# Kernel optimization log

Measured on AMD Instinct MI355X. Metric: run time of the kernel, lower is better.

Reference implementation:

```python
import jax, jax.numpy as jnp
import numpy as np


def setup_inputs() -> dict:
    key = jax.random.key(0)
    kq, kk, kv = jax.random.split(key, 3)
    B, H, S, D = 4, 16, 2048, 64
    q = jax.random.normal(kq, (B, H, S, D), dtype=jnp.float32)
    k = jax.random.normal(kk, (B, H, S, D), dtype=jnp.float32)
    v = jax.random.normal(kv, (B, H, S, D), dtype=jnp.float32)
    return {"q": q, "k": k, "v": v}


def reference(q, k, v):
    # SplitScaleAttend (inference, no mask, no dropout):
    # softmax(q k^T / sqrt(d)) v — the chunked loop in the original is a
    # memory-saving schedule of the same math, so one fused expression here.
    scale = q.shape[-1] ** (-0.5)
    # (b h i d),(b h j d) -> (b h i j)
    sim = jnp.einsum("bhid,bhjd->bhij", q, k * scale)
    attn = jax.nn.softmax(sim, axis=-1)
    # (b h i j),(b h j d) -> (b h i d)
    return jnp.einsum("bhij,bhjd->bhid", attn, v)
```

## Files before the change

kernel.cpp:

```cpp
#include <hip/hip_runtime.h>
#include <hip/hip_bf16.h>

typedef __attribute__((ext_vector_type(8))) short short8_t;
typedef __attribute__((ext_vector_type(4))) float f32x4;
typedef __attribute__((ext_vector_type(16))) float f32x16;
typedef __attribute__((ext_vector_type(4))) unsigned u32x4;

static constexpr int B = 4, H = 16, S = 2048, D = 64;
static constexpr int WAVES = 8, QW = 32, QBLK = WAVES * QW;
static constexpr int KVBLK = 64, NT = S / KVBLK;
static constexpr int LDK = 72;

#define QSCALE 0.18033688011112042f

__device__ __forceinline__ unsigned pk2(float a, float b) {
    __hip_bfloat162 h = __float22bfloat162_rn(float2{a, b});
    unsigned u;
    __builtin_memcpy(&u, &h, 4);
    return u;
}

__device__ __forceinline__ float fexp2(float x) {
#if __has_builtin(__builtin_amdgcn_exp2f)
    return __builtin_amdgcn_exp2f(x);
#else
    return exp2f(x);
#endif
}

__device__ __forceinline__ float frcp(float x) {
#if __has_builtin(__builtin_amdgcn_rcpf)
    return __builtin_amdgcn_rcpf(x);
#else
    return 1.f / x;
#endif
}

#define PV_STEP(CD, H, KS)                                                               \
    do {                                                                                 \
        unsigned x0 = CD[4 * (H) + 0], y0 = CD[4 * (H) + 2];                             \
        unsigned x1 = CD[4 * (H) + 1], y1 = CD[4 * (H) + 3];                             \
        asm volatile("v_permlane32_swap_b32 %0, %1" : "+v"(x0), "+v"(y0));               \
        asm volatile("v_permlane32_swap_b32 %0, %1" : "+v"(x1), "+v"(y1));               \
        const u32x4 pu = {x0, x1, y0, y1};                                               \
        const short8_t pa = __builtin_bit_cast(short8_t, pu);                            \
        const short8_t vfa =                                                             \
            *reinterpret_cast<const short8_t*>(&Vt[cb][ql][(KS) * 16 + hi * 8]);         \
        const short8_t vfb =                                                             \
            *reinterpret_cast<const short8_t*>(&Vt[cb][32 + ql][(KS) * 16 + hi * 8]);    \
        Od0 = __builtin_amdgcn_mfma_f32_32x32x16_bf16(pa, vfa, Od0, 0, 0, 0);            \
        Od1 = __builtin_amdgcn_mfma_f32_32x32x16_bf16(pa, vfb, Od1, 0, 0, 0);            \
        Ol  = __builtin_amdgcn_mfma_f32_32x32x16_bf16(pa, onesf, Ol, 0, 0, 0);           \
    } while (0)

__global__ void __launch_bounds__(512, 2)
attn_fwd(const float* __restrict__ q, const float* __restrict__ k,
         const float* __restrict__ v, float* __restrict__ out) {
    __shared__ short Ks[2][KVBLK][LDK];
    __shared__ short Vt[2][D][LDK];

    const int tid  = threadIdx.x;
    const int lane = tid & 63;
    const int ql   = lane & 31;
    const int hi   = lane >> 5;
    const int wave = tid >> 6;

    const long base = (long)blockIdx.y * S * D;
    const int  q0w  = blockIdx.x * QBLK + wave * QW;

    const u32x4 ones_u = {0x3F803F80u, 0x3F803F80u, 0x3F803F80u, 0x3F803F80u};
    const short8_t onesf = __builtin_bit_cast(short8_t, ones_u);

    short8_t qf[4];
    {
        const float* qp = q + base + (long)(q0w + ql) * D;
        #pragma unroll
        for (int kc = 0; kc < 4; ++kc) {
            const f32x4 a = *reinterpret_cast<const f32x4*>(qp + kc * 16 + hi * 8);
            const f32x4 b = *reinterpret_cast<const f32x4*>(qp + kc * 16 + hi * 8 + 4);
            const u32x4 u = {pk2(a[0] * QSCALE, a[1] * QSCALE),
                             pk2(a[2] * QSCALE, a[3] * QSCALE),
                             pk2(b[0] * QSCALE, b[1] * QSCALE),
                             pk2(b[2] * QSCALE, b[3] * QSCALE)};
            qf[kc] = __builtin_bit_cast(short8_t, u);
        }
    }

    f32x16 Od0, Od1, Ol;
    #pragma unroll
    for (int r = 0; r < 16; ++r) { Od0[r] = 0.f; Od1[r] = 0.f; Ol[r] = 0.f; }

    const int kr  = tid >> 3,       kc0 = (tid & 7) * 8;
    const int vk2 = (tid & 31) * 2, vd0 = (tid >> 5) * 4;
    const float* kptr  = k + base + (long)kr * D + kc0;
    const float* vptrA = v + base + (long)vk2 * D + vd0;
    const float* vptrB = vptrA + D;

    f32x4 kf0 = *reinterpret_cast<const f32x4*>(kptr);
    f32x4 kf1 = *reinterpret_cast<const f32x4*>(kptr + 4);
    f32x4 vfA = *reinterpret_cast<const f32x4*>(vptrA);
    f32x4 vfB = *reinterpret_cast<const f32x4*>(vptrB);

    for (int t = 0; t < NT; ++t) {
        const int cb = t & 1;
        {
            const u32x4 ku = {pk2(kf0[0], kf0[1]), pk2(kf0[2], kf0[3]),
                              pk2(kf1[0], kf1[1]), pk2(kf1[2], kf1[3])};
            *reinterpret_cast<u32x4*>(&Ks[cb][kr][kc0]) = ku;
            #pragma unroll
            for (int j = 0; j < 4; ++j) {
                const unsigned uv = pk2(vfA[j], vfB[j]);
                *reinterpret_cast<unsigned*>(&Vt[cb][vd0 + j][vk2]) = uv;
            }
        }
        if (t + 1 < NT) {
            kptr  += KVBLK * D;
            vptrA += KVBLK * D;
            vptrB += KVBLK * D;
            kf0 = *reinterpret_cast<const f32x4*>(kptr);
            kf1 = *reinterpret_cast<const f32x4*>(kptr + 4);
            vfA = *reinterpret_cast<const f32x4*>(vptrA);
            vfB = *reinterpret_cast<const f32x4*>(vptrB);
        }
        __syncthreads();

        f32x16 sA, sB;
        #pragma unroll
        for (int r = 0; r < 16; ++r) { sA[r] = 0.f; sB[r] = 0.f; }
        __builtin_amdgcn_s_setprio(1);
        #pragma unroll
        for (int kc = 0; kc < 4; ++kc) {
            const short8_t ka = *reinterpret_cast<const short8_t*>(&Ks[cb][ql][kc * 16 + hi * 8]);
            sA = __builtin_amdgcn_mfma_f32_32x32x16_bf16(ka, qf[kc], sA, 0, 0, 0);
        }
        #pragma unroll
        for (int kc = 0; kc < 4; ++kc) {
            const short8_t kb2 = *reinterpret_cast<const short8_t*>(&Ks[cb][32 + ql][kc * 16 + hi * 8]);
            sB = __builtin_amdgcn_mfma_f32_32x32x16_bf16(kb2, qf[kc], sB, 0, 0, 0);
        }
        __builtin_amdgcn_s_setprio(0);

        #pragma unroll
        for (int r = 0; r < 16; ++r) sA[r] = fexp2(sA[r]);
        #pragma unroll
        for (int r = 0; r < 16; ++r) sB[r] = fexp2(sB[r]);

        unsigned cdA[8], cdB[8];
        #pragma unroll
        for (int jj = 0; jj < 8; ++jj) {
            cdA[jj] = pk2(sA[jj * 2], sA[jj * 2 + 1]);
            cdB[jj] = pk2(sB[jj * 2], sB[jj * 2 + 1]);
        }

        __builtin_amdgcn_s_setprio(1);
        PV_STEP(cdA, 0, 0);
        PV_STEP(cdA, 1, 1);
        PV_STEP(cdB, 0, 2);
        PV_STEP(cdB, 1, 3);
        __builtin_amdgcn_s_setprio(0);
    }

    float* op = out + base + (long)q0w * D + ql;
    #pragma unroll
    for (int r = 0; r < 16; ++r) {
        const int   row = (r & 3) + 8 * (r >> 2) + 4 * hi;
        const float s   = frcp(Ol[r]);
        op[(long)row * D]      = Od0[r] * s;
        op[(long)row * D + 32] = Od1[r] * s;
    }
}

extern "C" void kernel_launch(void* const* d_in, const int* in_sizes, int n_in,
                              void* d_out, int out_size, void* d_ws, size_t ws_size,
                              hipStream_t stream) {
    const float* q = (const float*)d_in[0];
    const float* k = (const float*)d_in[1];
    const float* v = (const float*)d_in[2];
    float* out = (float*)d_out;
    dim3 grid(S / QBLK, B * H);
    attn_fwd<<<grid, 512, 0, stream>>>(q, k, v, out);
}
```

Baseline: 104.6 us.

## Process two 32-row query tiles per wave with four waves per block

Each wave now owns 64 query rows as two 32-row MFMA tiles, so each K and V fragment read from LDS is reused for both tiles, and the block drops to four waves. The loop is reordered so the next tile's global K/V loads are issued after the first QK half, and the QK/exp/PV work is split into two halves per KV tile. This halves LDS fragment traffic per query row and blocks per head stay the same. In exchange each wave holds twice as many accumulators, which raises register pressure, and there are fewer waves to hide latency.

```diff
diff --git a/kernel.cpp b/kernel.cpp
--- a/kernel.cpp
+++ b/kernel.cpp
@@ -7,7 +7,7 @@
 typedef __attribute__((ext_vector_type(4))) unsigned u32x4;
 
 static constexpr int B = 4, H = 16, S = 2048, D = 64;
-static constexpr int WAVES = 8, QW = 32, QBLK = WAVES * QW;
+static constexpr int WAVES = 4, QW = 64, QBLK = WAVES * QW;
 static constexpr int KVBLK = 64, NT = S / KVBLK;
 static constexpr int LDK = 72;
 
@@ -36,24 +36,63 @@
 #endif
 }
 
-#define PV_STEP(CD, H, KS)                                                               \
+#define PV2(CD0, CD1, KS)                                                                \
     do {                                                                                 \
-        unsigned x0 = CD[4 * (H) + 0], y0 = CD[4 * (H) + 2];                             \
-        unsigned x1 = CD[4 * (H) + 1], y1 = CD[4 * (H) + 3];                             \
-        asm volatile("v_permlane32_swap_b32 %0, %1" : "+v"(x0), "+v"(y0));               \
-        asm volatile("v_permlane32_swap_b32 %0, %1" : "+v"(x1), "+v"(y1));               \
-        const u32x4 pu = {x0, x1, y0, y1};                                               \
-        const short8_t pa = __builtin_bit_cast(short8_t, pu);                            \
+        const int h_ = (KS) & 1;                                                         \
         const short8_t vfa =                                                             \
             *reinterpret_cast<const short8_t*>(&Vt[cb][ql][(KS) * 16 + hi * 8]);         \
         const short8_t vfb =                                                             \
             *reinterpret_cast<const short8_t*>(&Vt[cb][32 + ql][(KS) * 16 + hi * 8]);    \
-        Od0 = __builtin_amdgcn_mfma_f32_32x32x16_bf16(pa, vfa, Od0, 0, 0, 0);            \
-        Od1 = __builtin_amdgcn_mfma_f32_32x32x16_bf16(pa, vfb, Od1, 0, 0, 0);            \
-        Ol  = __builtin_amdgcn_mfma_f32_32x32x16_bf16(pa, onesf, Ol, 0, 0, 0);           \
+        {                                                                                \
+            unsigned x0 = CD0[4 * h_ + 0], y0 = CD0[4 * h_ + 2];                         \
+            unsigned x1 = CD0[4 * h_ + 1], y1 = CD0[4 * h_ + 3];                         \
+            asm volatile("v_permlane32_swap_b32 %0, %1" : "+v"(x0), "+v"(y0));           \
+            asm volatile("v_permlane32_swap_b32 %0, %1" : "+v"(x1), "+v"(y1));           \
+            const u32x4 pu = {x0, x1, y0, y1};                                           \
+            const short8_t pa = __builtin_bit_cast(short8_t, pu);                        \
+            Od00 = __builtin_amdgcn_mfma_f32_32x32x16_bf16(pa, vfa, Od00, 0, 0, 0);      \
+            Od01 = __builtin_amdgcn_mfma_f32_32x32x16_bf16(pa, vfb, Od01, 0, 0, 0);      \
+            Ol0  = __builtin_amdgcn_mfma_f32_32x32x16_bf16(pa, onesf, Ol0, 0, 0, 0);     \
+        }                                                                                \
+        {                                                                                \
+            unsigned x0 = CD1[4 * h_ + 0], y0 = CD1[4 * h_ + 2];                         \
+            unsigned x1 = CD1[4 * h_ + 1], y1 = CD1[4 * h_ + 3];                         \
+            asm volatile("v_permlane32_swap_b32 %0, %1" : "+v"(x0), "+v"(y0));           \
+            asm volatile("v_permlane32_swap_b32 %0, %1" : "+v"(x1), "+v"(y1));           \
+            const u32x4 pu = {x0, x1, y0, y1};                                           \
+            const short8_t pa = __builtin_bit_cast(short8_t, pu);                        \
+            Od10 = __builtin_amdgcn_mfma_f32_32x32x16_bf16(pa, vfa, Od10, 0, 0, 0);      \
+            Od11 = __builtin_amdgcn_mfma_f32_32x32x16_bf16(pa, vfb, Od11, 0, 0, 0);      \
+            Ol1  = __builtin_amdgcn_mfma_f32_32x32x16_bf16(pa, onesf, Ol1, 0, 0, 0);     \
+        }                                                                                \
     } while (0)
 
-__global__ void __launch_bounds__(512, 2)
+#define QK_HALF(KH, CD0, CD1)                                                            \
+    do {                                                                                 \
+        f32x16 s0, s1;                                                                   \
+        _Pragma("unroll")                                                                \
+        for (int r = 0; r < 16; ++r) { s0[r] = 0.f; s1[r] = 0.f; }                       \
+        __builtin_amdgcn_s_setprio(1);                                                   \
+        _Pragma("unroll")                                                                \
+        for (int kc = 0; kc < 4; ++kc) {                                                 \
+            const short8_t ka = *reinterpret_cast<const short8_t*>(                      \
+                &Ks[cb][(KH) * 32 + ql][kc * 16 + hi * 8]);                              \
+            s0 = __builtin_amdgcn_mfma_f32_32x32x16_bf16(ka, qf0[kc], s0, 0, 0, 0);      \
+            s1 = __builtin_amdgcn_mfma_f32_32x32x16_bf16(ka, qf1[kc], s1, 0, 0, 0);      \
+        }                                                                                \
+        __builtin_amdgcn_s_setprio(0);                                                   \
+        _Pragma("unroll")                                                                \
+        for (int r = 0; r < 16; ++r) s0[r] = fexp2(s0[r]);                               \
+        _Pragma("unroll")                                                                \
+        for (int r = 0; r < 16; ++r) s1[r] = fexp2(s1[r]);                               \
+        _Pragma("unroll")                                                                \
+        for (int jj = 0; jj < 8; ++jj) {                                                 \
+            CD0[jj] = pk2(s0[jj * 2], s0[jj * 2 + 1]);                                   \
+            CD1[jj] = pk2(s1[jj * 2], s1[jj * 2 + 1]);                                   \
+        }                                                                                \
+    } while (0)
+
+__global__ void __launch_bounds__(256, 2)
 attn_fwd(const float* __restrict__ q, const float* __restrict__ k,
          const float* __restrict__ v, float* __restrict__ out) {
     __shared__ short Ks[2][KVBLK][LDK];
@@ -71,9 +110,10 @@
     const u32x4 ones_u = {0x3F803F80u, 0x3F803F80u, 0x3F803F80u, 0x3F803F80u};
     const short8_t onesf = __builtin_bit_cast(short8_t, ones_u);
 
-    short8_t qf[4];
-    {
-        const float* qp = q + base + (long)(q0w + ql) * D;
+    short8_t qf0[4], qf1[4];
+    #pragma unroll
+    for (int qb = 0; qb < 2; ++qb) {
+        const float* qp = q + base + (long)(q0w + qb * 32 + ql) * D;
         #pragma unroll
         for (int kc = 0; kc < 4; ++kc) {
             const f32x4 a = *reinterpret_cast<const f32x4*>(qp + kc * 16 + hi * 8);
@@ -82,91 +122,95 @@
                              pk2(a[2] * QSCALE, a[3] * QSCALE),
                              pk2(b[0] * QSCALE, b[1] * QSCALE),
                              pk2(b[2] * QSCALE, b[3] * QSCALE)};
-            qf[kc] = __builtin_bit_cast(short8_t, u);
-        }
-    }
-
-    f32x16 Od0, Od1, Ol;
+            if (qb == 0) qf0[kc] = __builtin_bit_cast(short8_t, u);
+            else         qf1[kc] = __builtin_bit_cast(short8_t, u);
+        }
+    }
+
+    f32x16 Od00, Od01, Ol0, Od10, Od11, Ol1;
     #pragma unroll
-    for (int r = 0; r < 16; ++r) { Od0[r] = 0.f; Od1[r] = 0.f; Ol[r] = 0.f; }
-
-    const int kr  = tid >> 3,       kc0 = (tid & 7) * 8;
-    const int vk2 = (tid & 31) * 2, vd0 = (tid >> 5) * 4;
+    for (int r = 0; r < 16; ++r) {
+        Od00[r] = 0.f; Od01[r] = 0.f; Ol0[r] = 0.f;
+        Od10[r] = 0.f; Od11[r] = 0.f; Ol1[r] = 0.f;
+    }
+
+    const int kr  = tid >> 2,       kc0 = (tid & 3) * 16;
+    const int vk2 = (tid & 31) * 2, vd0 = (tid >> 5) * 8;
     const float* kptr  = k + base + (long)kr * D + kc0;
     const float* vptrA = v + base + (long)vk2 * D + vd0;
-    const float* vptrB = vptrA + D;
-
-    f32x4 kf0 = *reinterpret_cast<const f32x4*>(kptr);
-    f32x4 kf1 = *reinterpret_cast<const f32x4*>(kptr + 4);
-    f32x4 vfA = *reinterpret_cast<const f32x4*>(vptrA);
-    f32x4 vfB = *reinterpret_cast<const f32x4*>(vptrB);
+
+    f32x4 kfa = *reinterpret_cast<const f32x4*>(kptr);
+    f32x4 kfb = *reinterpret_cast<const f32x4*>(kptr + 4);
+    f32x4 kfc = *reinterpret_cast<const f32x4*>(kptr + 8);
+    f32x4 kfd = *reinterpret_cast<const f32x4*>(kptr + 12);
+    f32x4 vfa0 = *reinterpret_cast<const f32x4*>(vptrA);
+    f32x4 vfa1 = *reinterpret_cast<const f32x4*>(vptrA + 4);
+    f32x4 vfb0 = *reinterpret_cast<const f32x4*>(vptrA + D);
+    f32x4 vfb1 = *reinterpret_cast<const f32x4*>(vptrA + D + 4);
 
     for (int t = 0; t < NT; ++t) {
         const int cb = t & 1;
         {
-            const u32x4 ku = {pk2(kf0[0], kf0[1]), pk2(kf0[2], kf0[3]),
-                              pk2(kf1[0], kf1[1]), pk2(kf1[2], kf1[3])};
-            *reinterpret_cast<u32x4*>(&Ks[cb][kr][kc0]) = ku;
+            const u32x4 ku0 = {pk2(kfa[0], kfa[1]), pk2(kfa[2], kfa[3]),
+                               pk2(kfb[0], kfb[1]), pk2(kfb[2], kfb[3])};
+            const u32x4 ku1 = {pk2(kfc[0], kfc[1]), pk2(kfc[2], kfc[3]),
+                               pk2(kfd[0], kfd[1]), pk2(kfd[2], kfd[3])};
+            *reinterpret_cast<u32x4*>(&Ks[cb][kr][kc0])     = ku0;
+            *reinterpret_cast<u32x4*>(&Ks[cb][kr][kc0 + 8]) = ku1;
             #pragma unroll
             for (int j = 0; j < 4; ++j) {
-                const unsigned uv = pk2(vfA[j], vfB[j]);
-                *reinterpret_cast<unsigned*>(&Vt[cb][vd0 + j][vk2]) = uv;
+                *reinterpret_cast<unsigned*>(&Vt[cb][vd0 + j][vk2])     = pk2(vfa0[j], vfb0[j]);
+                *reinterpret_cast<unsigned*>(&Vt[cb][vd0 + 4 + j][vk2]) = pk2(vfa1[j], vfb1[j]);
             }
         }
+        __syncthreads();
+
+        unsigned cd0[8], cd1[8];
+
+        QK_HALF(0, cd0, cd1);
+
         if (t + 1 < NT) {
             kptr  += KVBLK * D;
             vptrA += KVBLK * D;
-            vptrB += KVBLK * D;
-            kf0 = *reinterpret_cast<const f32x4*>(kptr);
-            kf1 = *reinterpret_cast<const f32x4*>(kptr + 4);
-            vfA = *reinterpret_cast<const f32x4*>(vptrA);
-            vfB = *reinterpret_cast<const f32x4*>(vptrB);
-        }
-        __syncthreads();
-
-        f32x16 sA, sB;
+            kfa = *reinterpret_cast<const f32x4*>(kptr);
+            kfb = *reinterpret_cast<const f32x4*>(kptr + 4);
+            kfc = *reinterpret_cast<const f32x4*>(kptr + 8);
+            kfd = *reinterpret_cast<const f32x4*>(kptr + 12);
+            vfa0 = *reinterpret_cast<const f32x4*>(vptrA);
+            vfa1 = *reinterpret_cast<const f32x4*>(vptrA + 4);
+            vfb0 = *reinterpret_cast<const f32x4*>(vptrA + D);
+            vfb1 = *reinterpret_cast<const f32x4*>(vptrA + D + 4);
+        }
+
+        __builtin_amdgcn_s_setprio(1);
+        PV2(cd0, cd1, 0);
+        PV2(cd0, cd1, 1);
+        __builtin_amdgcn_s_setprio(0);
+
+        QK_HALF(1, cd0, cd1);
+        __builtin_amdgcn_s_setprio(1);
+        PV2(cd0, cd1, 2);
+        PV2(cd0, cd1, 3);
+        __builtin_amdgcn_s_setprio(0);
+    }
+
+    {
+        float* op = out + base + (long)q0w * D + ql;
         #pragma unroll
-        for (int r = 0; r < 16; ++r) { sA[r] = 0.f; sB[r] = 0.f; }
-        __builtin_amdgcn_s_setprio(1);
+        for (int r = 0; r < 16; ++r) {
+            const int   row = (r & 3) + 8 * (r >> 2) + 4 * hi;
+            const float s   = frcp(Ol0[r]);
+            op[(long)row * D]      = Od00[r] * s;
+            op[(long)row * D + 32] = Od01[r] * s;
+        }
+        float* op1 = op + 32 * D;
         #pragma unroll
-        for (int kc = 0; kc < 4; ++kc) {
-            const short8_t ka = *reinterpret_cast<const short8_t*>(&Ks[cb][ql][kc * 16 + hi * 8]);
-            sA = __builtin_amdgcn_mfma_f32_32x32x16_bf16(ka, qf[kc], sA, 0, 0, 0);
-        }
-        #pragma unroll
-        for (int kc = 0; kc < 4; ++kc) {
-            const short8_t kb2 = *reinterpret_cast<const short8_t*>(&Ks[cb][32 + ql][kc * 16 + hi * 8]);
-            sB = __builtin_amdgcn_mfma_f32_32x32x16_bf16(kb2, qf[kc], sB, 0, 0, 0);
-        }
-        __builtin_amdgcn_s_setprio(0);
-
-        #pragma unroll
-        for (int r = 0; r < 16; ++r) sA[r] = fexp2(sA[r]);
-        #pragma unroll
-        for (int r = 0; r < 16; ++r) sB[r] = fexp2(sB[r]);
-
-        unsigned cdA[8], cdB[8];
-        #pragma unroll
-        for (int jj = 0; jj < 8; ++jj) {
-            cdA[jj] = pk2(sA[jj * 2], sA[jj * 2 + 1]);
-            cdB[jj] = pk2(sB[jj * 2], sB[jj * 2 + 1]);
-        }
-
-        __builtin_amdgcn_s_setprio(1);
-        PV_STEP(cdA, 0, 0);
-        PV_STEP(cdA, 1, 1);
-        PV_STEP(cdB, 0, 2);
-        PV_STEP(cdB, 1, 3);
-        __builtin_amdgcn_s_setprio(0);
-    }
-
-    float* op = out + base + (long)q0w * D + ql;
-    #pragma unroll
-    for (int r = 0; r < 16; ++r) {
-        const int   row = (r & 3) + 8 * (r >> 2) + 4 * hi;
-        const float s   = frcp(Ol[r]);
-        op[(long)row * D]      = Od0[r] * s;
-        op[(long)row * D + 32] = Od1[r] * s;
+        for (int r = 0; r < 16; ++r) {
+            const int   row = (r & 3) + 8 * (r >> 2) + 4 * hi;
+            const float s   = frcp(Ol1[r]);
+            op1[(long)row * D]      = Od10[r] * s;
+            op1[(long)row * D + 32] = Od11[r] * s;
+        }
     }
 }
 
@@ -178,5 +222,5 @@
     const float* v = (const float*)d_in[2];
     float* out = (float*)d_out;
     dim3 grid(S / QBLK, B * H);
-    attn_fwd<<<grid, 512, 0, stream>>>(q, k, v, out);
-}
+    attn_fwd<<<grid, 256, 0, stream>>>(q, k, v, out);
+}
```

Result: faster. 101.1 us (-3.4%).

## Shrink blocks to 4 waves, swizzle grid order, and split QK/PV into halves

Applied to the files above, without the earlier changes.

Cuts each workgroup from 8 waves to 4, so each block handles 128 queries. Each thread now stages twice as much K/V per tile, and launch bounds are raised to allow 4 blocks per CU. The launch becomes a 1D grid with a swizzle that places 8 consecutive blocks on different heads, to spread K/V reads for L2 locality. The QK and softmax-PV work is processed in two 32-key halves to reduce live score registers, and the prefetch of the next tile moves after the barrier. The cost is that K/V staging is duplicated across twice as many blocks, which raises global and LDS traffic per query.

```diff
diff --git a/kernel.cpp b/kernel.cpp
--- a/kernel.cpp
+++ b/kernel.cpp
@@ -7,7 +7,7 @@
 typedef __attribute__((ext_vector_type(4))) unsigned u32x4;
 
 static constexpr int B = 4, H = 16, S = 2048, D = 64;
-static constexpr int WAVES = 8, QW = 32, QBLK = WAVES * QW;
+static constexpr int WAVES = 4, QW = 32, QBLK = WAVES * QW;
 static constexpr int KVBLK = 64, NT = S / KVBLK;
 static constexpr int LDK = 72;
 
@@ -36,24 +36,25 @@
 #endif
 }
 
-#define PV_STEP(CD, H, KS)                                                               \
+#define PV2(CD, KS)                                                                      \
     do {                                                                                 \
-        unsigned x0 = CD[4 * (H) + 0], y0 = CD[4 * (H) + 2];                             \
-        unsigned x1 = CD[4 * (H) + 1], y1 = CD[4 * (H) + 3];                             \
+        const int h_ = (KS) & 1;                                                         \
+        const short8_t vfa =                                                             \
+            *reinterpret_cast<const short8_t*>(&Vt[cb][ql][(KS) * 16 + hi * 8]);         \
+        const short8_t vfb =                                                             \
+            *reinterpret_cast<const short8_t*>(&Vt[cb][32 + ql][(KS) * 16 + hi * 8]);    \
+        unsigned x0 = CD[4 * h_ + 0], y0 = CD[4 * h_ + 2];                               \
+        unsigned x1 = CD[4 * h_ + 1], y1 = CD[4 * h_ + 3];                               \
         asm volatile("v_permlane32_swap_b32 %0, %1" : "+v"(x0), "+v"(y0));               \
         asm volatile("v_permlane32_swap_b32 %0, %1" : "+v"(x1), "+v"(y1));               \
         const u32x4 pu = {x0, x1, y0, y1};                                               \
         const short8_t pa = __builtin_bit_cast(short8_t, pu);                            \
-        const short8_t vfa =                                                             \
-            *reinterpret_cast<const short8_t*>(&Vt[cb][ql][(KS) * 16 + hi * 8]);         \
-        const short8_t vfb =                                                             \
-            *reinterpret_cast<const short8_t*>(&Vt[cb][32 + ql][(KS) * 16 + hi * 8]);    \
         Od0 = __builtin_amdgcn_mfma_f32_32x32x16_bf16(pa, vfa, Od0, 0, 0, 0);            \
         Od1 = __builtin_amdgcn_mfma_f32_32x32x16_bf16(pa, vfb, Od1, 0, 0, 0);            \
         Ol  = __builtin_amdgcn_mfma_f32_32x32x16_bf16(pa, onesf, Ol, 0, 0, 0);           \
     } while (0)
 
-__global__ void __launch_bounds__(512, 2)
+__global__ void __launch_bounds__(256, 4)
 attn_fwd(const float* __restrict__ q, const float* __restrict__ k,
          const float* __restrict__ v, float* __restrict__ out) {
     __shared__ short Ks[2][KVBLK][LDK];
@@ -63,10 +64,13 @@
     const int lane = tid & 63;
     const int ql   = lane & 31;
     const int hi   = lane >> 5;
-    const int wave = tid >> 6;
 
-    const long base = (long)blockIdx.y * S * D;
-    const int  q0w  = blockIdx.x * QBLK + wave * QW;
+    const int lid = blockIdx.x;
+    const int bh  = (lid & 7) | ((lid >> 7) << 3);
+    const int qx  = (lid >> 3) & 15;
+
+    const long base = (long)bh * S * D;
+    const int  q0w  = qx * QBLK + (tid >> 6) * QW;
 
     const u32x4 ones_u = {0x3F803F80u, 0x3F803F80u, 0x3F803F80u, 0x3F803F80u};
     const short8_t onesf = __builtin_bit_cast(short8_t, ones_u);
@@ -90,74 +94,75 @@
     #pragma unroll
     for (int r = 0; r < 16; ++r) { Od0[r] = 0.f; Od1[r] = 0.f; Ol[r] = 0.f; }
 
-    const int kr  = tid >> 3,       kc0 = (tid & 7) * 8;
-    const int vk2 = (tid & 31) * 2, vd0 = (tid >> 5) * 4;
+    const int kr  = tid >> 2,       kc0 = (tid & 3) * 16;
+    const int vk2 = (tid & 31) * 2, vd0 = (tid >> 5) * 8;
     const float* kptr  = k + base + (long)kr * D + kc0;
     const float* vptrA = v + base + (long)vk2 * D + vd0;
-    const float* vptrB = vptrA + D;
 
-    f32x4 kf0 = *reinterpret_cast<const f32x4*>(kptr);
-    f32x4 kf1 = *reinterpret_cast<const f32x4*>(kptr + 4);
-    f32x4 vfA = *reinterpret_cast<const f32x4*>(vptrA);
-    f32x4 vfB = *reinterpret_cast<const f32x4*>(vptrB);
+    f32x4 kfa = *reinterpret_cast<const f32x4*>(kptr);
+    f32x4 kfb = *reinterpret_cast<const f32x4*>(kptr + 4);
+    f32x4 kfc = *reinterpret_cast<const f32x4*>(kptr + 8);
+    f32x4 kfd = *reinterpret_cast<const f32x4*>(kptr + 12);
+    f32x4 vfa0 = *reinterpret_cast<const f32x4*>(vptrA);
+    f32x4 vfa1 = *reinterpret_cast<const f32x4*>(vptrA + 4);
+    f32x4 vfb0 = *reinterpret_cast<const f32x4*>(vptrA + D);
+    f32x4 vfb1 = *reinterpret_cast<const f32x4*>(vptrA + D + 4);
 
     for (int t = 0; t < NT; ++t) {
         const int cb = t & 1;
         {
-            const u32x4 ku = {pk2(kf0[0], kf0[1]), pk2(kf0[2], kf0[3]),
-                              pk2(kf1[0], kf1[1]), pk2(kf1[2], kf1[3])};
-            *reinterpret_cast<u32x4*>(&Ks[cb][kr][kc0]) = ku;
+            const u32x4 ku0 = {pk2(kfa[0], kfa[1]), pk2(kfa[2], kfa[3]),
+                               pk2(kfb[0], kfb[1]), pk2(kfb[2], kfb[3])};
+            const u32x4 ku1 = {pk2(kfc[0], kfc[1]), pk2(kfc[2], kfc[3]),
+                               pk2(kfd[0], kfd[1]), pk2(kfd[2], kfd[3])};
+            *reinterpret_cast<u32x4*>(&Ks[cb][kr][kc0])     = ku0;
+            *reinterpret_cast<u32x4*>(&Ks[cb][kr][kc0 + 8]) = ku1;
             #pragma unroll
             for (int j = 0; j < 4; ++j) {
-                const unsigned uv = pk2(vfA[j], vfB[j]);
-                *reinterpret_cast<unsigned*>(&Vt[cb][vd0 + j][vk2]) = uv;
+                *reinterpret_cast<unsigned*>(&Vt[cb][vd0 + j][vk2])     = pk2(vfa0[j], vfb0[j]);
+                *reinterpret_cast<unsigned*>(&Vt[cb][vd0 + 4 + j][vk2]) = pk2(vfa1[j], vfb1[j]);
             }
         }
+        __syncthreads();
+
         if (t + 1 < NT) {
             kptr  += KVBLK * D;
             vptrA += KVBLK * D;
-            vptrB += KVBLK * D;
-            kf0 = *reinterpret_cast<const f32x4*>(kptr);
-            kf1 = *reinterpret_cast<const f32x4*>(kptr + 4);
-            vfA = *reinterpret_cast<const f32x4*>(vptrA);
-            vfB = *reinterpret_cast<const f32x4*>(vptrB);
+            kfa = *reinterpret_cast<const f32x4*>(kptr);
+            kfb = *reinterpret_cast<const f32x4*>(kptr + 4);
+            kfc = *reinterpret_cast<const f32x4*>(kptr + 8);
+            kfd = *reinterpret_cast<const f32x4*>(kptr + 12);
+            vfa0 = *reinterpret_cast<const f32x4*>(vptrA);
+            vfa1 = *reinterpret_cast<const f32x4*>(vptrA + 4);
+            vfb0 = *reinterpret_cast<const f32x4*>(vptrA + D);
+            vfb1 = *reinterpret_cast<const f32x4*>(vptrA + D + 4);
         }
-        __syncthreads();
-
-        f32x16 sA, sB;
-        #pragma unroll
-        for (int r = 0; r < 16; ++r) { sA[r] = 0.f; sB[r] = 0.f; }
-        __builtin_amdgcn_s_setprio(1);
-        #pragma unroll
-        for (int kc = 0; kc < 4; ++kc) {
-            const short8_t ka = *reinterpret_cast<const short8_t*>(&Ks[cb][ql][kc * 16 + hi * 8]);
-            sA = __builtin_amdgcn_mfma_f32_32x32x16_bf16(ka, qf[kc], sA, 0, 0, 0);
-        }
-        #pragma unroll
-        for (int kc = 0; kc < 4; ++kc) {
-            const short8_t kb2 = *reinterpret_cast<const short8_t*>(&Ks[cb][32 + ql][kc * 16 + hi * 8]);
-            sB = __builtin_amdgcn_mfma_f32_32x32x16_bf16(kb2, qf[kc], sB, 0, 0, 0);
-        }
-        __builtin_amdgcn_s_setprio(0);
 
         #pragma unroll
-        for (int r = 0; r < 16; ++r) sA[r] = fexp2(sA[r]);
-        #pragma unroll
-        for (int r = 0; r < 16; ++r) sB[r] = fexp2(sB[r]);
+        for (int kh = 0; kh < 2; ++kh) {
+            f32x16 s;
+            #pragma unroll
+            for (int r = 0; r < 16; ++r) s[r] = 0.f;
+            __builtin_amdgcn_s_setprio(1);
+            #pragma unroll
+            for (int kc = 0; kc < 4; ++kc) {
+                const short8_t ka = *reinterpret_cast<const short8_t*>(
+                    &Ks[cb][kh * 32 + ql][kc * 16 + hi * 8]);
+                s = __builtin_amdgcn_mfma_f32_32x32x16_bf16(ka, qf[kc], s, 0, 0, 0);
+            }
+            __builtin_amdgcn_s_setprio(0);
 
-        unsigned cdA[8], cdB[8];
-        #pragma unroll
-        for (int jj = 0; jj < 8; ++jj) {
-            cdA[jj] = pk2(sA[jj * 2], sA[jj * 2 + 1]);
-            cdB[jj] = pk2(sB[jj * 2], sB[jj * 2 + 1]);
+            #pragma unroll
+            for (int r = 0; r < 16; ++r) s[r] = fexp2(s[r]);
+            unsigned cd[8];
+            #pragma unroll
+            for (int jj = 0; jj < 8; ++jj) cd[jj] = pk2(s[jj * 2], s[jj * 2 + 1]);
+
+            __builtin_amdgcn_s_setprio(1);
+            PV2(cd, 2 * kh);
+            PV2(cd, 2 * kh + 1);
+            __builtin_amdgcn_s_setprio(0);
         }
-
-        __builtin_amdgcn_s_setprio(1);
-        PV_STEP(cdA, 0, 0);
-        PV_STEP(cdA, 1, 1);
-        PV_STEP(cdB, 0, 2);
-        PV_STEP(cdB, 1, 3);
-        __builtin_amdgcn_s_setprio(0);
     }
 
     float* op = out + base + (long)q0w * D + ql;
@@ -177,6 +182,5 @@
     const float* k = (const float*)d_in[1];
     const float* v = (const float*)d_in[2];
     float* out = (float*)d_out;
-    dim3 grid(S / QBLK, B * H);
-    attn_fwd<<<grid, 512, 0, stream>>>(q, k, v, out);
+    attn_fwd<<<dim3((S / QBLK) * B * H), 256, 0, stream>>>(q, k, v, out);
 }
```

Measured after the change: 140.2 us (median of 2 runs). +34.0%, slower.
